# Optimization experiments

Measured on AMD Instinct MI355X. Metric: run time of the kernel, lower is better.

The kernel has to match this reference:

```python
import jax, jax.numpy as jnp
import numpy as np

HIDDEN = 4096
K = 4          # Gibbs sampling steps
LR = 0.01
IMG = (16, 64, 64, 3)  # batch, H, W, C


def setup_inputs() -> dict:
    key = jax.random.key(0)
    k1, k2 = jax.random.split(key)
    inputs = jax.random.uniform(k1, IMG, dtype=jnp.float32)
    flat = IMG[1] * IMG[2] * IMG[3]
    # GlorotNormal init: std = sqrt(2 / (fan_in + fan_out))
    scale = (2.0 / (flat + HIDDEN)) ** 0.5
    W = jax.random.normal(k2, (flat, HIDDEN), dtype=jnp.float32) * scale
    a = jnp.zeros((flat, 1), dtype=jnp.float32)
    b = jnp.zeros((HIDDEN, 1), dtype=jnp.float32)
    return {"inputs": inputs, "W": W, "a": a, "b": b}


def reference(inputs, W, a, b):
    B = inputs.shape[0]
    flat = inputs.shape[1] * inputs.shape[2] * inputs.shape[3]
    vs = inputs.reshape(B, flat, 1)  # each sample is a (flat,1) column vector

    def per_sample(carry, v):
        W, a, b = carry
        v_init = v
        # k Gibbs steps: h = sigma(b + W^T v); v = sigma(a + W h)
        h = None
        for _ in range(K):
            h = jax.nn.sigmoid(b + W.T @ v)
            v = jax.nn.sigmoid(a + W @ h)
        h_init = jax.nn.sigmoid(b + W.T @ v_init)
        # Contrastive divergence with .assign (replace, not accumulate) as in source
        W_new = LR * (v_init @ h_init.T - v @ h.T)
        a_new = LR * (v_init - v)
        b_new = LR * (h_init - h)
        return (W_new, a_new, b_new), v

    _, vs_out = jax.lax.scan(per_sample, (W, a, b), vs)
    # call() returns self.v, i.e. the reconstruction of the LAST batch element
    return vs_out[-1]
```

## Files before the change

### kernel.cpp

```cpp
#include <hip/hip_runtime.h>
#include <math.h>

#define FLAT 12288
#define NH   4096
#define KSTEPS 4
#define LRC 0.01f
#define NSEG 384
#define RPS  32
#define NSEG2 768
#define WSCALE 64.0f
#define WINV   0.015625f

typedef float v2f __attribute__((ext_vector_type(2)));

__device__ __forceinline__ float sigm(float x) {
    return __builtin_amdgcn_rcpf(1.0f + __expf(-x));
}

template <int CTRL>
__device__ __forceinline__ float dpp_add(float x) {
    int s = __builtin_amdgcn_update_dpp(0, __float_as_int(x), CTRL, 0xf, 0xf, true);
    return x + __int_as_float(s);
}
__device__ __forceinline__ float wave_sum63(float x) {
    x = dpp_add<0x111>(x);
    x = dpp_add<0x112>(x);
    x = dpp_add<0x114>(x);
    x = dpp_add<0x118>(x);
    x = dpp_add<0x142>(x);
    x = dpp_add<0x143>(x);
    return x;
}


__global__ __launch_bounds__(256) void k_colpart_cvt(const float* __restrict__ W,
                                                     const float* __restrict__ v,
                                                     float* __restrict__ partials,
                                                     unsigned int* __restrict__ W8) {
    const float4* W4 = (const float4*)W;
    int c4 = blockIdx.x * 256 + threadIdx.x;
    int r0 = blockIdx.y * RPS;
    float4 acc = make_float4(0.f, 0.f, 0.f, 0.f);
    for (int r = r0; r < r0 + RPS; ++r) {
        float vr = v[r];
        float4 w = W4[(size_t)r * (NH / 4) + c4];
        acc.x = fmaf(w.x, vr, acc.x);
        acc.y = fmaf(w.y, vr, acc.y);
        acc.z = fmaf(w.z, vr, acc.z);
        acc.w = fmaf(w.w, vr, acc.w);
        unsigned int p = 0;
        p = __builtin_amdgcn_cvt_pk_fp8_f32(w.x * WSCALE, w.y * WSCALE, p, false);
        p = __builtin_amdgcn_cvt_pk_fp8_f32(w.z * WSCALE, w.w * WSCALE, p, true);
        W8[(size_t)r * (NH / 4) + c4] = p;
    }
    ((float4*)partials)[(size_t)blockIdx.y * (NH / 4) + c4] = acc;
}

__global__ __launch_bounds__(256) void k_hreduce(const float* __restrict__ partials,
                                                 const float* __restrict__ b,
                                                 float* __restrict__ h,
                                                 float* __restrict__ hi,
                                                 int nseg) {
    int c  = threadIdx.x & 31;
    int sg = threadIdx.x >> 5;
    int col = blockIdx.x * 32 + c;
    float s = 0.f;
    for (int g = sg; g < nseg; g += 8) s += partials[(size_t)g * NH + col];
    __shared__ float red[8][33];
    red[sg][c] = s;
    __syncthreads();
    if (threadIdx.x < 32) {
        float t = 0.f;
#pragma unroll
        for (int g2 = 0; g2 < 8; g2++) t += red[g2][threadIdx.x];
        float hh = sigm(t + b[col]);
        h[col] = hh;
        if (hi) hi[col] = hh;
    }
}

__global__ __launch_bounds__(256, 1) void k_fused(const unsigned char* __restrict__ W8,
                                                  const float* __restrict__ h,
                                                  const float* __restrict__ a,
                                                  float* __restrict__ v,
                                                  float* __restrict__ partials) {
    int lane = threadIdx.x & 63, wv = threadIdx.x >> 6;
    int rbase = blockIdx.x * 64 + wv * 16;
    const float4* h4 = (const float4*)h;

    float4 hreg[16];
#pragma unroll
    for (int j = 0; j < 4; j++) {
        int k = lane + 64 * j;
#pragma unroll
        for (int q = 0; q < 4; q++) hreg[4 * j + q] = h4[4 * k + q];
    }

    float pacc[64];
#pragma unroll
    for (int i = 0; i < 64; i++) pacc[i] = 0.f;

    for (int i = 0; i < 16; ++i) {
        int r = rbase + i;
        const uint4* Wr = (const uint4*)(W8 + (size_t)r * NH);
        uint4 wq[4];
#pragma unroll
        for (int j = 0; j < 4; j++) wq[j] = Wr[lane + 64 * j];

        float dot = 0.f;
#pragma unroll
        for (int j = 0; j < 4; j++) {
            v2f f;
            f = __builtin_amdgcn_cvt_pk_f32_fp8(wq[j].x, false); dot = fmaf(f.x, hreg[4*j].x, dot);   dot = fmaf(f.y, hreg[4*j].y, dot);
            f = __builtin_amdgcn_cvt_pk_f32_fp8(wq[j].x, true);  dot = fmaf(f.x, hreg[4*j].z, dot);   dot = fmaf(f.y, hreg[4*j].w, dot);
            f = __builtin_amdgcn_cvt_pk_f32_fp8(wq[j].y, false); dot = fmaf(f.x, hreg[4*j+1].x, dot); dot = fmaf(f.y, hreg[4*j+1].y, dot);
            f = __builtin_amdgcn_cvt_pk_f32_fp8(wq[j].y, true);  dot = fmaf(f.x, hreg[4*j+1].z, dot); dot = fmaf(f.y, hreg[4*j+1].w, dot);
            f = __builtin_amdgcn_cvt_pk_f32_fp8(wq[j].z, false); dot = fmaf(f.x, hreg[4*j+2].x, dot); dot = fmaf(f.y, hreg[4*j+2].y, dot);
            f = __builtin_amdgcn_cvt_pk_f32_fp8(wq[j].z, true);  dot = fmaf(f.x, hreg[4*j+2].z, dot); dot = fmaf(f.y, hreg[4*j+2].w, dot);
            f = __builtin_amdgcn_cvt_pk_f32_fp8(wq[j].w, false); dot = fmaf(f.x, hreg[4*j+3].x, dot); dot = fmaf(f.y, hreg[4*j+3].y, dot);
            f = __builtin_amdgcn_cvt_pk_f32_fp8(wq[j].w, true);  dot = fmaf(f.x, hreg[4*j+3].z, dot); dot = fmaf(f.y, hreg[4*j+3].w, dot);
        }
        dot = wave_sum63(dot);
        float full = __shfl(dot, 63);
        float vr = sigm(a[r] + full * WINV);
        if (lane == 63) v[r] = vr;

        float vs = vr * WINV;
#pragma unroll
        for (int j = 0; j < 4; j++) {
            v2f f;
            f = __builtin_amdgcn_cvt_pk_f32_fp8(wq[j].x, false); pacc[16*j+0]  = fmaf(f.x, vs, pacc[16*j+0]);  pacc[16*j+1]  = fmaf(f.y, vs, pacc[16*j+1]);
            f = __builtin_amdgcn_cvt_pk_f32_fp8(wq[j].x, true);  pacc[16*j+2]  = fmaf(f.x, vs, pacc[16*j+2]);  pacc[16*j+3]  = fmaf(f.y, vs, pacc[16*j+3]);
            f = __builtin_amdgcn_cvt_pk_f32_fp8(wq[j].y, false); pacc[16*j+4]  = fmaf(f.x, vs, pacc[16*j+4]);  pacc[16*j+5]  = fmaf(f.y, vs, pacc[16*j+5]);
            f = __builtin_amdgcn_cvt_pk_f32_fp8(wq[j].y, true);  pacc[16*j+6]  = fmaf(f.x, vs, pacc[16*j+6]);  pacc[16*j+7]  = fmaf(f.y, vs, pacc[16*j+7]);
            f = __builtin_amdgcn_cvt_pk_f32_fp8(wq[j].z, false); pacc[16*j+8]  = fmaf(f.x, vs, pacc[16*j+8]);  pacc[16*j+9]  = fmaf(f.y, vs, pacc[16*j+9]);
            f = __builtin_amdgcn_cvt_pk_f32_fp8(wq[j].z, true);  pacc[16*j+10] = fmaf(f.x, vs, pacc[16*j+10]); pacc[16*j+11] = fmaf(f.y, vs, pacc[16*j+11]);
            f = __builtin_amdgcn_cvt_pk_f32_fp8(wq[j].w, false); pacc[16*j+12] = fmaf(f.x, vs, pacc[16*j+12]); pacc[16*j+13] = fmaf(f.y, vs, pacc[16*j+13]);
            f = __builtin_amdgcn_cvt_pk_f32_fp8(wq[j].w, true);  pacc[16*j+14] = fmaf(f.x, vs, pacc[16*j+14]); pacc[16*j+15] = fmaf(f.y, vs, pacc[16*j+15]);
        }
    }

    float* P = partials + (size_t)(blockIdx.x * 4 + wv) * NH;
#pragma unroll
    for (int j = 0; j < 4; j++) {
        float4* Pj = (float4*)(P + 16 * (lane + 64 * j));
#pragma unroll
        for (int q = 0; q < 4; q++) {
            float4 o;
            o.x = pacc[16*j + 4*q + 0]; o.y = pacc[16*j + 4*q + 1];
            o.z = pacc[16*j + 4*q + 2]; o.w = pacc[16*j + 4*q + 3];
            Pj[q] = o;
        }
    }
}

__global__ __launch_bounds__(256) void k_vstep_fp8(const unsigned char* __restrict__ W8,
                                                   const float* __restrict__ h,
                                                   const float* __restrict__ a,
                                                   float* __restrict__ v) {
    int wid = threadIdx.x >> 6, lane = threadIdx.x & 63;
    int row = blockIdx.x * 4 + wid;
    const uint4* Wr = (const uint4*)(W8 + (size_t)row * NH);
    const float4* h4 = (const float4*)h;
    float acc = 0.f;
    for (int k = lane; k < NH / 16; k += 64) {
        uint4 w = Wr[k];
        float4 h0 = h4[4*k], h1 = h4[4*k+1], h2 = h4[4*k+2], h3 = h4[4*k+3];
        v2f f;
        f = __builtin_amdgcn_cvt_pk_f32_fp8(w.x, false); acc = fmaf(f.x, h0.x, acc); acc = fmaf(f.y, h0.y, acc);
        f = __builtin_amdgcn_cvt_pk_f32_fp8(w.x, true);  acc = fmaf(f.x, h0.z, acc); acc = fmaf(f.y, h0.w, acc);
        f = __builtin_amdgcn_cvt_pk_f32_fp8(w.y, false); acc = fmaf(f.x, h1.x, acc); acc = fmaf(f.y, h1.y, acc);
        f = __builtin_amdgcn_cvt_pk_f32_fp8(w.y, true);  acc = fmaf(f.x, h1.z, acc); acc = fmaf(f.y, h1.w, acc);
        f = __builtin_amdgcn_cvt_pk_f32_fp8(w.z, false); acc = fmaf(f.x, h2.x, acc); acc = fmaf(f.y, h2.y, acc);
        f = __builtin_amdgcn_cvt_pk_f32_fp8(w.z, true);  acc = fmaf(f.x, h2.z, acc); acc = fmaf(f.y, h2.w, acc);
        f = __builtin_amdgcn_cvt_pk_f32_fp8(w.w, false); acc = fmaf(f.x, h3.x, acc); acc = fmaf(f.y, h3.y, acc);
        f = __builtin_amdgcn_cvt_pk_f32_fp8(w.w, true);  acc = fmaf(f.x, h3.z, acc); acc = fmaf(f.y, h3.w, acc);
    }
    acc = wave_sum63(acc);
    if (lane == 63) v[row] = sigm(a[row] + acc * WINV);
}


#define TB  512
#define RVB (FLAT / TB)
#define RHB (NH / TB)
#define NWAVES (TB / 64)

__global__ __launch_bounds__(512) void k_phaseB(const float* __restrict__ inputs,
                                                const float* __restrict__ hi0,
                                                const float* __restrict__ hk0,
                                                const float* __restrict__ vk0,
                                                float* __restrict__ out) {
    int t = threadIdx.x;
    int lane = t & 63, wid = t >> 6;
    __shared__ float2 red[2][NWAVES];

    float Vi[RVB], Vk[RVB], v[RVB];
    float Hi[RHB], Hk[RHB], h[RHB], hini[RHB];

#pragma unroll
    for (int r = 0; r < RVB; r++) { int i = r * TB + t; Vi[r] = inputs[i]; Vk[r] = vk0[i]; }
#pragma unroll
    for (int r = 0; r < RHB; r++) { int j = r * TB + t; Hi[r] = hi0[j]; Hk[r] = hk0[j]; }

    int rc = 0;
    for (int s = 1; s < 16; ++s) {
        const float* vin = inputs + (size_t)s * FLAT;
#pragma unroll
        for (int r = 0; r < RVB; r++) v[r] = vin[r * TB + t];

        for (int k = 0; k < KSTEPS; ++k) {
            float px0 = 0.f, px1 = 0.f, py0 = 0.f, py1 = 0.f;
#pragma unroll
            for (int r = 0; r < RVB; r += 2) {
                px0 = fmaf(Vi[r],   v[r],   px0); py0 = fmaf(Vk[r],   v[r],   py0);
                px1 = fmaf(Vi[r+1], v[r+1], px1); py1 = fmaf(Vk[r+1], v[r+1], py1);
            }
            float px = wave_sum63(px0 + px1), py = wave_sum63(py0 + py1);
            if (lane == 63) { float2 w2; w2.x = px; w2.y = py; red[rc & 1][wid] = w2; }
            __syncthreads();
            float al = 0.f, be = 0.f;
#pragma unroll
            for (int w = 0; w < NWAVES; w++) { float2 w2 = red[rc & 1][w]; al += w2.x; be += w2.y; }
            rc++;
            float ca = LRC * (1.f + al), cb = LRC * (1.f + be);

            float qx = 0.f, qy = 0.f;
#pragma unroll
            for (int r = 0; r < RHB; r++) {
                float hh = sigm(ca * Hi[r] - cb * Hk[r]);
                h[r] = hh;
                if (k == 0) hini[r] = hh;
                qx = fmaf(Hi[r], hh, qx); qy = fmaf(Hk[r], hh, qy);
            }
            qx = wave_sum63(qx); qy = wave_sum63(qy);
            if (lane == 63) { float2 w2; w2.x = qx; w2.y = qy; red[rc & 1][wid] = w2; }
            __syncthreads();
            float ga = 0.f, de = 0.f;
#pragma unroll
            for (int w = 0; w < NWAVES; w++) { float2 w2 = red[rc & 1][w]; ga += w2.x; de += w2.y; }
            rc++;
            float cg = LRC * (1.f + ga), cd = LRC * (1.f + de);

#pragma unroll
            for (int r = 0; r < RVB; r++) v[r] = sigm(cg * Vi[r] - cd * Vk[r]);
        }

#pragma unroll
        for (int r = 0; r < RVB; r++) { Vk[r] = v[r]; Vi[r] = vin[r * TB + t]; }
#pragma unroll
        for (int r = 0; r < RHB; r++) { Hk[r] = h[r]; Hi[r] = hini[r]; }
    }

#pragma unroll
    for (int r = 0; r < RVB; r++) out[r * TB + t] = Vk[r];
}


extern "C" void kernel_launch(void* const* d_in, const int* in_sizes, int n_in,
                              void* d_out, int out_size, void* d_ws, size_t ws_size,
                              hipStream_t stream) {
    const float* inputs = (const float*)d_in[0];
    const float* W      = (const float*)d_in[1];
    const float* a_in   = (const float*)d_in[2];
    const float* b_in   = (const float*)d_in[3];
    float* out = (float*)d_out;

    unsigned int* W8 = (unsigned int*)d_ws;
    float* partials = (float*)((char*)d_ws + (size_t)FLAT * NH);
    float* h  = partials + (size_t)NSEG2 * NH;
    float* hi = h + NH;
    float* v  = hi + NH;

    dim3 blk(256);

    k_colpart_cvt<<<dim3(4, NSEG), blk, 0, stream>>>(W, inputs, partials, W8);
    k_hreduce<<<dim3(NH / 32), blk, 0, stream>>>(partials, b_in, h, hi, NSEG);

    for (int k = 1; k < KSTEPS; ++k) {
        k_fused<<<dim3(FLAT / 64), blk, 0, stream>>>((const unsigned char*)W8, h, a_in, v, partials);
        k_hreduce<<<dim3(NH / 32), blk, 0, stream>>>(partials, b_in, h, (float*)nullptr, NSEG2);
    }
    k_vstep_fp8<<<dim3(FLAT / 4), blk, 0, stream>>>((const unsigned char*)W8, h, a_in, v);

    k_phaseB<<<1, TB, 0, stream>>>(inputs, hi, h, v, out);
}
```

Before: 546.5 us.

## Fuse all stages into one persistent cooperative kernel with grid syncs

Replaces the chain of separate launches (column partials with FP8 conversion, h reductions, fused v/h steps, final v step, serial phase B) with one cooperative kernel of 256 blocks that uses grid.sync between stages. Per-wave partial accumulators are combined in shared memory with atomics, so each block writes one partial row and the h reduction reads 256 segments instead of 768. This removes launch gaps and cuts partial traffic. In exchange, the whole grid must stay co-resident, occupancy is fixed at 256 blocks, and the long single-block phase B now runs inside the big kernel.

```diff
diff --git a/kernel.cpp b/kernel.cpp
--- a/kernel.cpp
+++ b/kernel.cpp
@@ -1,15 +1,21 @@
 #include <hip/hip_runtime.h>
+#include <hip/hip_cooperative_groups.h>
 #include <math.h>
+
+namespace cg = cooperative_groups;
 
 #define FLAT 12288
 #define NH   4096
 #define KSTEPS 4
 #define LRC 0.01f
-#define NSEG 384
-#define RPS  32
-#define NSEG2 768
 #define WSCALE 64.0f
 #define WINV   0.015625f
+
+#define NBLK 256
+#define TPB  512
+#define ROWS_PER_BLK 48
+#define ROWS_PER_WAVE 6
+#define NSEGP NBLK
 
 typedef float v2f __attribute__((ext_vector_type(2)));
 
@@ -32,228 +38,227 @@
     return x;
 }
 
-
-__global__ __launch_bounds__(256) void k_colpart_cvt(const float* __restrict__ W,
-                                                     const float* __restrict__ v,
-                                                     float* __restrict__ partials,
-                                                     unsigned int* __restrict__ W8) {
-    const float4* W4 = (const float4*)W;
-    int c4 = blockIdx.x * 256 + threadIdx.x;
-    int r0 = blockIdx.y * RPS;
-    float4 acc = make_float4(0.f, 0.f, 0.f, 0.f);
-    for (int r = r0; r < r0 + RPS; ++r) {
-        float vr = v[r];
-        float4 w = W4[(size_t)r * (NH / 4) + c4];
-        acc.x = fmaf(w.x, vr, acc.x);
-        acc.y = fmaf(w.y, vr, acc.y);
-        acc.z = fmaf(w.z, vr, acc.z);
-        acc.w = fmaf(w.w, vr, acc.w);
-        unsigned int p = 0;
-        p = __builtin_amdgcn_cvt_pk_fp8_f32(w.x * WSCALE, w.y * WSCALE, p, false);
-        p = __builtin_amdgcn_cvt_pk_fp8_f32(w.z * WSCALE, w.w * WSCALE, p, true);
-        W8[(size_t)r * (NH / 4) + c4] = p;
-    }
-    ((float4*)partials)[(size_t)blockIdx.y * (NH / 4) + c4] = acc;
-}
-
-__global__ __launch_bounds__(256) void k_hreduce(const float* __restrict__ partials,
-                                                 const float* __restrict__ b,
-                                                 float* __restrict__ h,
-                                                 float* __restrict__ hi,
-                                                 int nseg) {
-    int c  = threadIdx.x & 31;
-    int sg = threadIdx.x >> 5;
-    int col = blockIdx.x * 32 + c;
-    float s = 0.f;
-    for (int g = sg; g < nseg; g += 8) s += partials[(size_t)g * NH + col];
-    __shared__ float red[8][33];
-    red[sg][c] = s;
-    __syncthreads();
-    if (threadIdx.x < 32) {
-        float t = 0.f;
-#pragma unroll
-        for (int g2 = 0; g2 < 8; g2++) t += red[g2][threadIdx.x];
-        float hh = sigm(t + b[col]);
-        h[col] = hh;
-        if (hi) hi[col] = hh;
-    }
-}
-
-__global__ __launch_bounds__(256, 1) void k_fused(const unsigned char* __restrict__ W8,
-                                                  const float* __restrict__ h,
-                                                  const float* __restrict__ a,
-                                                  float* __restrict__ v,
-                                                  float* __restrict__ partials) {
-    int lane = threadIdx.x & 63, wv = threadIdx.x >> 6;
-    int rbase = blockIdx.x * 64 + wv * 16;
-    const float4* h4 = (const float4*)h;
-
-    float4 hreg[16];
+__device__ __forceinline__ float dot64(const uint4* wq, const float4* hreg) {
+    float d0 = 0.f, d1 = 0.f, d2 = 0.f, d3 = 0.f;
 #pragma unroll
     for (int j = 0; j < 4; j++) {
-        int k = lane + 64 * j;
-#pragma unroll
-        for (int q = 0; q < 4; q++) hreg[4 * j + q] = h4[4 * k + q];
-    }
-
-    float pacc[64];
-#pragma unroll
-    for (int i = 0; i < 64; i++) pacc[i] = 0.f;
-
-    for (int i = 0; i < 16; ++i) {
-        int r = rbase + i;
-        const uint4* Wr = (const uint4*)(W8 + (size_t)r * NH);
-        uint4 wq[4];
-#pragma unroll
-        for (int j = 0; j < 4; j++) wq[j] = Wr[lane + 64 * j];
-
-        float dot = 0.f;
-#pragma unroll
-        for (int j = 0; j < 4; j++) {
-            v2f f;
-            f = __builtin_amdgcn_cvt_pk_f32_fp8(wq[j].x, false); dot = fmaf(f.x, hreg[4*j].x, dot);   dot = fmaf(f.y, hreg[4*j].y, dot);
-            f = __builtin_amdgcn_cvt_pk_f32_fp8(wq[j].x, true);  dot = fmaf(f.x, hreg[4*j].z, dot);   dot = fmaf(f.y, hreg[4*j].w, dot);
-            f = __builtin_amdgcn_cvt_pk_f32_fp8(wq[j].y, false); dot = fmaf(f.x, hreg[4*j+1].x, dot); dot = fmaf(f.y, hreg[4*j+1].y, dot);
-            f = __builtin_amdgcn_cvt_pk_f32_fp8(wq[j].y, true);  dot = fmaf(f.x, hreg[4*j+1].z, dot); dot = fmaf(f.y, hreg[4*j+1].w, dot);
-            f = __builtin_amdgcn_cvt_pk_f32_fp8(wq[j].z, false); dot = fmaf(f.x, hreg[4*j+2].x, dot); dot = fmaf(f.y, hreg[4*j+2].y, dot);
-            f = __builtin_amdgcn_cvt_pk_f32_fp8(wq[j].z, true);  dot = fmaf(f.x, hreg[4*j+2].z, dot); dot = fmaf(f.y, hreg[4*j+2].w, dot);
-            f = __builtin_amdgcn_cvt_pk_f32_fp8(wq[j].w, false); dot = fmaf(f.x, hreg[4*j+3].x, dot); dot = fmaf(f.y, hreg[4*j+3].y, dot);
-            f = __builtin_amdgcn_cvt_pk_f32_fp8(wq[j].w, true);  dot = fmaf(f.x, hreg[4*j+3].z, dot); dot = fmaf(f.y, hreg[4*j+3].w, dot);
-        }
-        dot = wave_sum63(dot);
-        float full = __shfl(dot, 63);
-        float vr = sigm(a[r] + full * WINV);
-        if (lane == 63) v[r] = vr;
-
-        float vs = vr * WINV;
-#pragma unroll
-        for (int j = 0; j < 4; j++) {
-            v2f f;
-            f = __builtin_amdgcn_cvt_pk_f32_fp8(wq[j].x, false); pacc[16*j+0]  = fmaf(f.x, vs, pacc[16*j+0]);  pacc[16*j+1]  = fmaf(f.y, vs, pacc[16*j+1]);
-            f = __builtin_amdgcn_cvt_pk_f32_fp8(wq[j].x, true);  pacc[16*j+2]  = fmaf(f.x, vs, pacc[16*j+2]);  pacc[16*j+3]  = fmaf(f.y, vs, pacc[16*j+3]);
-            f = __builtin_amdgcn_cvt_pk_f32_fp8(wq[j].y, false); pacc[16*j+4]  = fmaf(f.x, vs, pacc[16*j+4]);  pacc[16*j+5]  = fmaf(f.y, vs, pacc[16*j+5]);
-            f = __builtin_amdgcn_cvt_pk_f32_fp8(wq[j].y, true);  pacc[16*j+6]  = fmaf(f.x, vs, pacc[16*j+6]);  pacc[16*j+7]  = fmaf(f.y, vs, pacc[16*j+7]);
-            f = __builtin_amdgcn_cvt_pk_f32_fp8(wq[j].z, false); pacc[16*j+8]  = fmaf(f.x, vs, pacc[16*j+8]);  pacc[16*j+9]  = fmaf(f.y, vs, pacc[16*j+9]);
-            f = __builtin_amdgcn_cvt_pk_f32_fp8(wq[j].z, true);  pacc[16*j+10] = fmaf(f.x, vs, pacc[16*j+10]); pacc[16*j+11] = fmaf(f.y, vs, pacc[16*j+11]);
-            f = __builtin_amdgcn_cvt_pk_f32_fp8(wq[j].w, false); pacc[16*j+12] = fmaf(f.x, vs, pacc[16*j+12]); pacc[16*j+13] = fmaf(f.y, vs, pacc[16*j+13]);
-            f = __builtin_amdgcn_cvt_pk_f32_fp8(wq[j].w, true);  pacc[16*j+14] = fmaf(f.x, vs, pacc[16*j+14]); pacc[16*j+15] = fmaf(f.y, vs, pacc[16*j+15]);
-        }
-    }
-
-    float* P = partials + (size_t)(blockIdx.x * 4 + wv) * NH;
+        v2f f;
+        f = __builtin_amdgcn_cvt_pk_f32_fp8(wq[j].x, false); d0 = fmaf(f.x, hreg[4*j+0].x, d0); d1 = fmaf(f.y, hreg[4*j+0].y, d1);
+        f = __builtin_amdgcn_cvt_pk_f32_fp8(wq[j].x, true);  d2 = fmaf(f.x, hreg[4*j+0].z, d2); d3 = fmaf(f.y, hreg[4*j+0].w, d3);
+        f = __builtin_amdgcn_cvt_pk_f32_fp8(wq[j].y, false); d0 = fmaf(f.x, hreg[4*j+1].x, d0); d1 = fmaf(f.y, hreg[4*j+1].y, d1);
+        f = __builtin_amdgcn_cvt_pk_f32_fp8(wq[j].y, true);  d2 = fmaf(f.x, hreg[4*j+1].z, d2); d3 = fmaf(f.y, hreg[4*j+1].w, d3);
+        f = __builtin_amdgcn_cvt_pk_f32_fp8(wq[j].z, false); d0 = fmaf(f.x, hreg[4*j+2].x, d0); d1 = fmaf(f.y, hreg[4*j+2].y, d1);
+        f = __builtin_amdgcn_cvt_pk_f32_fp8(wq[j].z, true);  d2 = fmaf(f.x, hreg[4*j+2].z, d2); d3 = fmaf(f.y, hreg[4*j+2].w, d3);
+        f = __builtin_amdgcn_cvt_pk_f32_fp8(wq[j].w, false); d0 = fmaf(f.x, hreg[4*j+3].x, d0); d1 = fmaf(f.y, hreg[4*j+3].y, d1);
+        f = __builtin_amdgcn_cvt_pk_f32_fp8(wq[j].w, true);  d2 = fmaf(f.x, hreg[4*j+3].z, d2); d3 = fmaf(f.y, hreg[4*j+3].w, d3);
+    }
+    return (d0 + d1) + (d2 + d3);
+}
+
+__device__ __forceinline__ void pacc64(const uint4* wq, float vs, float* pacc) {
 #pragma unroll
     for (int j = 0; j < 4; j++) {
-        float4* Pj = (float4*)(P + 16 * (lane + 64 * j));
-#pragma unroll
-        for (int q = 0; q < 4; q++) {
-            float4 o;
-            o.x = pacc[16*j + 4*q + 0]; o.y = pacc[16*j + 4*q + 1];
-            o.z = pacc[16*j + 4*q + 2]; o.w = pacc[16*j + 4*q + 3];
-            Pj[q] = o;
-        }
-    }
-}
-
-__global__ __launch_bounds__(256) void k_vstep_fp8(const unsigned char* __restrict__ W8,
-                                                   const float* __restrict__ h,
-                                                   const float* __restrict__ a,
-                                                   float* __restrict__ v) {
-    int wid = threadIdx.x >> 6, lane = threadIdx.x & 63;
-    int row = blockIdx.x * 4 + wid;
-    const uint4* Wr = (const uint4*)(W8 + (size_t)row * NH);
-    const float4* h4 = (const float4*)h;
-    float acc = 0.f;
-    for (int k = lane; k < NH / 16; k += 64) {
-        uint4 w = Wr[k];
-        float4 h0 = h4[4*k], h1 = h4[4*k+1], h2 = h4[4*k+2], h3 = h4[4*k+3];
         v2f f;
-        f = __builtin_amdgcn_cvt_pk_f32_fp8(w.x, false); acc = fmaf(f.x, h0.x, acc); acc = fmaf(f.y, h0.y, acc);
-        f = __builtin_amdgcn_cvt_pk_f32_fp8(w.x, true);  acc = fmaf(f.x, h0.z, acc); acc = fmaf(f.y, h0.w, acc);
-        f = __builtin_amdgcn_cvt_pk_f32_fp8(w.y, false); acc = fmaf(f.x, h1.x, acc); acc = fmaf(f.y, h1.y, acc);
-        f = __builtin_amdgcn_cvt_pk_f32_fp8(w.y, true);  acc = fmaf(f.x, h1.z, acc); acc = fmaf(f.y, h1.w, acc);
-        f = __builtin_amdgcn_cvt_pk_f32_fp8(w.z, false); acc = fmaf(f.x, h2.x, acc); acc = fmaf(f.y, h2.y, acc);
-        f = __builtin_amdgcn_cvt_pk_f32_fp8(w.z, true);  acc = fmaf(f.x, h2.z, acc); acc = fmaf(f.y, h2.w, acc);
-        f = __builtin_amdgcn_cvt_pk_f32_fp8(w.w, false); acc = fmaf(f.x, h3.x, acc); acc = fmaf(f.y, h3.y, acc);
-        f = __builtin_amdgcn_cvt_pk_f32_fp8(w.w, true);  acc = fmaf(f.x, h3.z, acc); acc = fmaf(f.y, h3.w, acc);
-    }
-    acc = wave_sum63(acc);
-    if (lane == 63) v[row] = sigm(a[row] + acc * WINV);
-}
-
-
-#define TB  512
-#define RVB (FLAT / TB)
-#define RHB (NH / TB)
-#define NWAVES (TB / 64)
-
-__global__ __launch_bounds__(512) void k_phaseB(const float* __restrict__ inputs,
-                                                const float* __restrict__ hi0,
-                                                const float* __restrict__ hk0,
-                                                const float* __restrict__ vk0,
-                                                float* __restrict__ out) {
-    int t = threadIdx.x;
-    int lane = t & 63, wid = t >> 6;
-    __shared__ float2 red[2][NWAVES];
-
-    float Vi[RVB], Vk[RVB], v[RVB];
-    float Hi[RHB], Hk[RHB], h[RHB], hini[RHB];
-
-#pragma unroll
-    for (int r = 0; r < RVB; r++) { int i = r * TB + t; Vi[r] = inputs[i]; Vk[r] = vk0[i]; }
-#pragma unroll
-    for (int r = 0; r < RHB; r++) { int j = r * TB + t; Hi[r] = hi0[j]; Hk[r] = hk0[j]; }
-
-    int rc = 0;
-    for (int s = 1; s < 16; ++s) {
-        const float* vin = inputs + (size_t)s * FLAT;
-#pragma unroll
-        for (int r = 0; r < RVB; r++) v[r] = vin[r * TB + t];
-
-        for (int k = 0; k < KSTEPS; ++k) {
-            float px0 = 0.f, px1 = 0.f, py0 = 0.f, py1 = 0.f;
-#pragma unroll
-            for (int r = 0; r < RVB; r += 2) {
-                px0 = fmaf(Vi[r],   v[r],   px0); py0 = fmaf(Vk[r],   v[r],   py0);
-                px1 = fmaf(Vi[r+1], v[r+1], px1); py1 = fmaf(Vk[r+1], v[r+1], py1);
-            }
-            float px = wave_sum63(px0 + px1), py = wave_sum63(py0 + py1);
-            if (lane == 63) { float2 w2; w2.x = px; w2.y = py; red[rc & 1][wid] = w2; }
+        f = __builtin_amdgcn_cvt_pk_f32_fp8(wq[j].x, false); pacc[16*j+0]  = fmaf(f.x, vs, pacc[16*j+0]);  pacc[16*j+1]  = fmaf(f.y, vs, pacc[16*j+1]);
+        f = __builtin_amdgcn_cvt_pk_f32_fp8(wq[j].x, true);  pacc[16*j+2]  = fmaf(f.x, vs, pacc[16*j+2]);  pacc[16*j+3]  = fmaf(f.y, vs, pacc[16*j+3]);
+        f = __builtin_amdgcn_cvt_pk_f32_fp8(wq[j].y, false); pacc[16*j+4]  = fmaf(f.x, vs, pacc[16*j+4]);  pacc[16*j+5]  = fmaf(f.y, vs, pacc[16*j+5]);
+        f = __builtin_amdgcn_cvt_pk_f32_fp8(wq[j].y, true);  pacc[16*j+6]  = fmaf(f.x, vs, pacc[16*j+6]);  pacc[16*j+7]  = fmaf(f.y, vs, pacc[16*j+7]);
+        f = __builtin_amdgcn_cvt_pk_f32_fp8(wq[j].z, false); pacc[16*j+8]  = fmaf(f.x, vs, pacc[16*j+8]);  pacc[16*j+9]  = fmaf(f.y, vs, pacc[16*j+9]);
+        f = __builtin_amdgcn_cvt_pk_f32_fp8(wq[j].z, true);  pacc[16*j+10] = fmaf(f.x, vs, pacc[16*j+10]); pacc[16*j+11] = fmaf(f.y, vs, pacc[16*j+11]);
+        f = __builtin_amdgcn_cvt_pk_f32_fp8(wq[j].w, false); pacc[16*j+12] = fmaf(f.x, vs, pacc[16*j+12]); pacc[16*j+13] = fmaf(f.y, vs, pacc[16*j+13]);
+        f = __builtin_amdgcn_cvt_pk_f32_fp8(wq[j].w, true);  pacc[16*j+14] = fmaf(f.x, vs, pacc[16*j+14]); pacc[16*j+15] = fmaf(f.y, vs, pacc[16*j+15]);
+    }
+}
+
+#define RVB (FLAT / TPB)
+#define RHB (NH / TPB)
+
+__global__ __launch_bounds__(TPB) void k_all(const float* __restrict__ inputs,
+                                             const float* __restrict__ W,
+                                             const float* __restrict__ a_in,
+                                             const float* __restrict__ b_in,
+                                             float* __restrict__ out,
+                                             unsigned int* __restrict__ W8,
+                                             float* __restrict__ partials,
+                                             float* __restrict__ h,
+                                             float* __restrict__ hi,
+                                             float* __restrict__ v) {
+    cg::grid_group grid = cg::this_grid();
+    const int t = threadIdx.x, b = blockIdx.x;
+    const int lane = t & 63, wv = t >> 6;
+
+    __shared__ float  lred[NH];
+    __shared__ float  hred[16][33];
+    __shared__ float2 redB[2][8];
+
+    {
+        const float4* W4 = (const float4*)W;
+        const int r0 = b * ROWS_PER_BLK;
+        float4 acc0 = make_float4(0.f, 0.f, 0.f, 0.f);
+        float4 acc1 = make_float4(0.f, 0.f, 0.f, 0.f);
+        for (int r = r0; r < r0 + ROWS_PER_BLK; ++r) {
+            float vr = inputs[r];
+            float4 w0 = W4[(size_t)r * (NH / 4) + t];
+            float4 w1 = W4[(size_t)r * (NH / 4) + t + TPB];
+            acc0.x = fmaf(w0.x, vr, acc0.x); acc0.y = fmaf(w0.y, vr, acc0.y);
+            acc0.z = fmaf(w0.z, vr, acc0.z); acc0.w = fmaf(w0.w, vr, acc0.w);
+            acc1.x = fmaf(w1.x, vr, acc1.x); acc1.y = fmaf(w1.y, vr, acc1.y);
+            acc1.z = fmaf(w1.z, vr, acc1.z); acc1.w = fmaf(w1.w, vr, acc1.w);
+            unsigned int p0 = 0, p1 = 0;
+            p0 = __builtin_amdgcn_cvt_pk_fp8_f32(w0.x * WSCALE, w0.y * WSCALE, p0, false);
+            p0 = __builtin_amdgcn_cvt_pk_fp8_f32(w0.z * WSCALE, w0.w * WSCALE, p0, true);
+            p1 = __builtin_amdgcn_cvt_pk_fp8_f32(w1.x * WSCALE, w1.y * WSCALE, p1, false);
+            p1 = __builtin_amdgcn_cvt_pk_fp8_f32(w1.z * WSCALE, w1.w * WSCALE, p1, true);
+            W8[(size_t)r * (NH / 4) + t]       = p0;
+            W8[(size_t)r * (NH / 4) + t + TPB] = p1;
+        }
+        float4* P = (float4*)(partials + (size_t)b * NH);
+        P[t] = acc0;
+        P[t + TPB] = acc1;
+    }
+    grid.sync();
+
+    for (int step = 0; step < KSTEPS; ++step) {
+        {
+            int colg = t >> 5, s = t & 31;
+            int col = b * 16 + colg;
+            float sum = 0.f;
+            for (int g = s; g < NSEGP; g += 32) sum += partials[(size_t)g * NH + col];
+            hred[colg][s] = sum;
             __syncthreads();
-            float al = 0.f, be = 0.f;
-#pragma unroll
-            for (int w = 0; w < NWAVES; w++) { float2 w2 = red[rc & 1][w]; al += w2.x; be += w2.y; }
-            rc++;
-            float ca = LRC * (1.f + al), cb = LRC * (1.f + be);
-
-            float qx = 0.f, qy = 0.f;
-#pragma unroll
-            for (int r = 0; r < RHB; r++) {
-                float hh = sigm(ca * Hi[r] - cb * Hk[r]);
-                h[r] = hh;
-                if (k == 0) hini[r] = hh;
-                qx = fmaf(Hi[r], hh, qx); qy = fmaf(Hk[r], hh, qy);
-            }
-            qx = wave_sum63(qx); qy = wave_sum63(qy);
-            if (lane == 63) { float2 w2; w2.x = qx; w2.y = qy; red[rc & 1][wid] = w2; }
+            if (t < 16) {
+                int col2 = b * 16 + t;
+                float s2 = 0.f;
+#pragma unroll
+                for (int q = 0; q < 32; q++) s2 += hred[t][q];
+                float hh = sigm(s2 + b_in[col2]);
+                h[col2] = hh;
+                if (step == 0) hi[col2] = hh;
+            }
             __syncthreads();
-            float ga = 0.f, de = 0.f;
-#pragma unroll
-            for (int w = 0; w < NWAVES; w++) { float2 w2 = red[rc & 1][w]; ga += w2.x; de += w2.y; }
-            rc++;
-            float cg = LRC * (1.f + ga), cd = LRC * (1.f + de);
-
-#pragma unroll
-            for (int r = 0; r < RVB; r++) v[r] = sigm(cg * Vi[r] - cd * Vk[r]);
-        }
-
-#pragma unroll
-        for (int r = 0; r < RVB; r++) { Vk[r] = v[r]; Vi[r] = vin[r * TB + t]; }
-#pragma unroll
-        for (int r = 0; r < RHB; r++) { Hk[r] = h[r]; Hi[r] = hini[r]; }
-    }
-
-#pragma unroll
-    for (int r = 0; r < RVB; r++) out[r * TB + t] = Vk[r];
+        }
+        grid.sync();
+
+        const bool last = (step == KSTEPS - 1);
+
+        {
+            if (!last) {
+                for (int i = t; i < NH; i += TPB) lred[i] = 0.f;
+            }
+            const float4* h4 = (const float4*)h;
+            float4 hreg[16];
+#pragma unroll
+            for (int j = 0; j < 4; j++)
+#pragma unroll
+                for (int q = 0; q < 4; q++) hreg[4*j+q] = h4[4 * (lane + 64*j) + q];
+
+            if (!last) __syncthreads();
+
+            const uint4* W84 = (const uint4*)W8;
+            const int rbase = b * ROWS_PER_BLK + wv * ROWS_PER_WAVE;
+            float pacc[64];
+#pragma unroll
+            for (int i = 0; i < 64; i++) pacc[i] = 0.f;
+
+            for (int i = 0; i < ROWS_PER_WAVE; i += 2) {
+                int ra = rbase + i, rb = ra + 1;
+                uint4 wqa[4], wqb[4];
+#pragma unroll
+                for (int j = 0; j < 4; j++) {
+                    wqa[j] = W84[(size_t)ra * 256 + lane + 64*j];
+                    wqb[j] = W84[(size_t)rb * 256 + lane + 64*j];
+                }
+                float da = wave_sum63(dot64(wqa, hreg));
+                float db = wave_sum63(dot64(wqb, hreg));
+                float fa = __shfl(da, 63), fb = __shfl(db, 63);
+                float va = sigm(a_in[ra] + fa * WINV);
+                float vb = sigm(a_in[rb] + fb * WINV);
+                if (lane == 63) { v[ra] = va; v[rb] = vb; }
+                if (!last) {
+                    pacc64(wqa, va * WINV, pacc);
+                    pacc64(wqb, vb * WINV, pacc);
+                }
+            }
+
+            if (!last) {
+#pragma unroll
+                for (int j = 0; j < 4; j++)
+#pragma unroll
+                    for (int e = 0; e < 16; e++)
+                        atomicAdd(&lred[16 * (lane + 64*j) + e], pacc[16*j + e]);
+                __syncthreads();
+                float4* P = (float4*)(partials + (size_t)b * NH);
+                float4* L = (float4*)lred;
+                P[2*t]   = L[2*t];
+                P[2*t+1] = L[2*t+1];
+                __syncthreads();
+            }
+        }
+        grid.sync();
+    }
+
+    if (b != 0) return;
+    {
+        float Vi[RVB], Vk[RVB], vv[RVB];
+        float Hi[RHB], Hk[RHB], hh_[RHB], hini[RHB];
+
+#pragma unroll
+        for (int r = 0; r < RVB; r++) { int i = r * TPB + t; Vi[r] = inputs[i]; Vk[r] = v[i]; }
+#pragma unroll
+        for (int r = 0; r < RHB; r++) { int j = r * TPB + t; Hi[r] = hi[j]; Hk[r] = h[j]; }
+
+        int rc = 0;
+        for (int s = 1; s < 16; ++s) {
+            const float* vin = inputs + (size_t)s * FLAT;
+#pragma unroll
+            for (int r = 0; r < RVB; r++) vv[r] = vin[r * TPB + t];
+
+            for (int k = 0; k < KSTEPS; ++k) {
+                float px0 = 0.f, px1 = 0.f, py0 = 0.f, py1 = 0.f;
+#pragma unroll
+                for (int r = 0; r < RVB; r += 2) {
+                    px0 = fmaf(Vi[r],   vv[r],   px0); py0 = fmaf(Vk[r],   vv[r],   py0);
+                    px1 = fmaf(Vi[r+1], vv[r+1], px1); py1 = fmaf(Vk[r+1], vv[r+1], py1);
+                }
+                float px = wave_sum63(px0 + px1), py = wave_sum63(py0 + py1);
+                if (lane == 63) { float2 w2; w2.x = px; w2.y = py; redB[rc & 1][wv] = w2; }
+                __syncthreads();
+                float al = 0.f, be = 0.f;
+#pragma unroll
+                for (int w = 0; w < 8; w++) { float2 w2 = redB[rc & 1][w]; al += w2.x; be += w2.y; }
+                rc++;
+                float ca = LRC * (1.f + al), cb = LRC * (1.f + be);
+
+                float qx = 0.f, qy = 0.f;
+#pragma unroll
+                for (int r = 0; r < RHB; r++) {
+                    float hh = sigm(ca * Hi[r] - cb * Hk[r]);
+                    hh_[r] = hh;
+                    if (k == 0) hini[r] = hh;
+                    qx = fmaf(Hi[r], hh, qx); qy = fmaf(Hk[r], hh, qy);
+                }
+                qx = wave_sum63(qx); qy = wave_sum63(qy);
+                if (lane == 63) { float2 w2; w2.x = qx; w2.y = qy; redB[rc & 1][wv] = w2; }
+                __syncthreads();
+                float ga = 0.f, de = 0.f;
+#pragma unroll
+                for (int w = 0; w < 8; w++) { float2 w2 = redB[rc & 1][w]; ga += w2.x; de += w2.y; }
+                rc++;
+                float cg = LRC * (1.f + ga), cd = LRC * (1.f + de);
+
+#pragma unroll
+                for (int r = 0; r < RVB; r++) vv[r] = sigm(cg * Vi[r] - cd * Vk[r]);
+            }
+
+#pragma unroll
+            for (int r = 0; r < RVB; r++) { Vk[r] = vv[r]; Vi[r] = vin[r * TPB + t]; }
+#pragma unroll
+            for (int r = 0; r < RHB; r++) { Hk[r] = hh_[r]; Hi[r] = hini[r]; }
+        }
+
+#pragma unroll
+        for (int r = 0; r < RVB; r++) out[r * TPB + t] = Vk[r];
+    }
 }
 
 
@@ -268,20 +273,12 @@
 
     unsigned int* W8 = (unsigned int*)d_ws;
     float* partials = (float*)((char*)d_ws + (size_t)FLAT * NH);
-    float* h  = partials + (size_t)NSEG2 * NH;
+    float* h  = partials + (size_t)NSEGP * NH;
     float* hi = h + NH;
     float* v  = hi + NH;
 
-    dim3 blk(256);
-
-    k_colpart_cvt<<<dim3(4, NSEG), blk, 0, stream>>>(W, inputs, partials, W8);
-    k_hreduce<<<dim3(NH / 32), blk, 0, stream>>>(partials, b_in, h, hi, NSEG);
-
-    for (int k = 1; k < KSTEPS; ++k) {
-        k_fused<<<dim3(FLAT / 64), blk, 0, stream>>>((const unsigned char*)W8, h, a_in, v, partials);
-        k_hreduce<<<dim3(NH / 32), blk, 0, stream>>>(partials, b_in, h, (float*)nullptr, NSEG2);
-    }
-    k_vstep_fp8<<<dim3(FLAT / 4), blk, 0, stream>>>((const unsigned char*)W8, h, a_in, v);
-
-    k_phaseB<<<1, TB, 0, stream>>>(inputs, hi, h, v, out);
-}
+    void* args[] = {(void*)&inputs, (void*)&W, (void*)&a_in, (void*)&b_in,
+                    (void*)&out, (void*)&W8, (void*)&partials, (void*)&h,
+                    (void*)&hi, (void*)&v};
+    hipLaunchCooperativeKernel((void*)k_all, dim3(NBLK), dim3(TPB), args, 0, stream);
+}
```

Measured after the change: 876.2 us. 60.3% more time.
